# Performance work log

Hardware: AMD Instinct MI355X
Metric: run time of the kernel (lower is better)

Reference implementation:

```python
import jax, jax.numpy as jnp
import numpy as np

N, E, D, H, G, C = 100000, 1200000, 64, 64, 128, 10


def setup_inputs() -> dict:
    key = jax.random.key(0)
    ks = jax.random.split(key, 20)
    def lin(k, fin, fout):
        kw, kb = jax.random.split(k)
        s = 1.0 / np.sqrt(fin)
        return (jax.random.uniform(kw, (fin, fout), jnp.float32, -s, s),
                jax.random.uniform(kb, (fout,), jnp.float32, -s, s))
    w1a, b1a = lin(ks[0], D, H)
    w1b, b1b = lin(ks[1], H, H)
    w2a, b2a = lin(ks[2], H, H)
    w2b, b2b = lin(ks[3], H, H)
    w3a, b3a = lin(ks[4], H, H)
    w3b, b3b = lin(ks[5], H, H)
    wc, bc = lin(ks[6], H, C)
    x = jax.random.normal(ks[7], (N, D), jnp.float32)
    edge_index = jax.random.randint(ks[8], (2, E), 0, N, dtype=jnp.int32)
    batch = jnp.sort(jax.random.randint(ks[9], (N,), 0, G, dtype=jnp.int32))
    return {"x": x, "w1a": w1a, "b1a": b1a, "w1b": w1b, "b1b": b1b,
            "w2a": w2a, "b2a": b2a, "w2b": w2b, "b2b": b2b,
            "w3a": w3a, "b3a": b3a, "w3b": w3b, "b3b": b3b,
            "wc": wc, "bc": bc, "edge_index": edge_index, "batch": batch}


def _gin_layer(x, src, dst, wa, ba, wb, bb):
    # GINConv (eps=0): mlp(x + sum_{j in N(i)} x_j), then outer ReLU from GIN.forward
    agg = jax.ops.segment_sum(x[src], dst, num_segments=N)  # [N, d]
    h = x + agg
    h = jax.nn.relu(h @ wa + ba) @ wb + bb
    return jax.nn.relu(h)


def reference(x, w1a, b1a, w1b, b1b, w2a, b2a, w2b, b2b,
              w3a, b3a, w3b, b3b, wc, bc, edge_index, batch):
    src, dst = edge_index[0], edge_index[1]
    x = _gin_layer(x, src, dst, w1a, b1a, w1b, b1b)
    x = _gin_layer(x, src, dst, w2a, b2a, w2b, b2b)
    x = _gin_layer(x, src, dst, w3a, b3a, w3b, b3b)
    # global mean pool over graphs
    sums = jax.ops.segment_sum(x, batch, num_segments=G)              # [G, H]
    cnts = jax.ops.segment_sum(jnp.ones((N,), x.dtype), batch, num_segments=G)
    pooled = sums / jnp.maximum(cnts, 1.0)[:, None]
    return pooled @ wc + bc  # [G, C]
```

## Files before the change

### kernel.cpp

```cpp
#include <hip/hip_runtime.h>
#include <hip/hip_bf16.h>


#define N_NODES 100000
#define N_EDGES 1200000
#define N_GRAPH 128
#define N_CLS   10
#define NBUCK   391
#define BCAP    4096
#define BSH     12
#define HALFN   50000

typedef __bf16 bf16_t;
typedef __bf16 bf16x8 __attribute__((ext_vector_type(8)));
typedef float  f32x4  __attribute__((ext_vector_type(4)));

__global__ void tobf_kernel(const float* __restrict__ x, bf16_t* __restrict__ xb) {
    const int i = (blockIdx.x * 256 + threadIdx.x) * 8;
    const f32x4 a = *(const f32x4*)(x + i);
    const f32x4 b = *(const f32x4*)(x + i + 4);
    bf16x8 o;
#pragma unroll
    for (int j = 0; j < 4; ++j) { o[j] = (bf16_t)a[j]; o[4 + j] = (bf16_t)b[j]; }
    *(bf16x8*)(xb + i) = o;
}

__global__ void binA_kernel(const int* __restrict__ ei,
                            int* __restrict__ bcnt,
                            int* __restrict__ bpair) {
    __shared__ int lcnt[NBUCK];
    __shared__ int lbase[NBUCK];
    const int t = threadIdx.x;
    for (int b = t; b < NBUCK; b += 256) lcnt[b] = 0;
    __syncthreads();
    const int e0 = (blockIdx.x * 256 + t) * 4;
    int4 s4, d4; int b[4], r[4];
    const bool valid = e0 < N_EDGES;
    if (valid) {
        s4 = *(const int4*)(ei + e0);
        d4 = *(const int4*)(ei + N_EDGES + e0);
        b[0] = d4.x >> 8; b[1] = d4.y >> 8; b[2] = d4.z >> 8; b[3] = d4.w >> 8;
        r[0] = atomicAdd(&lcnt[b[0]], 1);
        r[1] = atomicAdd(&lcnt[b[1]], 1);
        r[2] = atomicAdd(&lcnt[b[2]], 1);
        r[3] = atomicAdd(&lcnt[b[3]], 1);
    }
    __syncthreads();
    for (int bb = t; bb < NBUCK; bb += 256) {
        const int c = lcnt[bb];
        lbase[bb] = c ? atomicAdd(&bcnt[bb], c) : 0;
    }
    __syncthreads();
    if (valid) {
        const int ss[4] = {s4.x, s4.y, s4.z, s4.w};
        const int dd[4] = {d4.x, d4.y, d4.z, d4.w};
#pragma unroll
        for (int j = 0; j < 4; ++j) {
            const int slot = lbase[b[j]] + r[j];
            if (slot < BCAP)
                bpair[(b[j] << BSH) + slot] = (ss[j] << 8) | (dd[j] & 255);
        }
    }
}

__global__ void bscan_kernel(const int* __restrict__ bcnt, int* __restrict__ cbase,
                             int* __restrict__ offset) {
    __shared__ int l[512];
    const int t = threadIdx.x;
    const int v = (t < NBUCK) ? bcnt[t] : 0;
    l[t] = v;
    __syncthreads();
    for (int d = 1; d < 512; d <<= 1) {
        int u = l[t];
        if (t >= d) u += l[t - d];
        __syncthreads();
        l[t] = u;
        __syncthreads();
    }
    if (t < NBUCK) cbase[t] = l[t] - v;
    if (t == NBUCK - 1) offset[N_NODES] = l[t];
}

__global__ void sortfill_kernel(const int* __restrict__ bpair,
                                const int* __restrict__ bcnt,
                                const int* __restrict__ cbase,
                                int* __restrict__ offset, int* __restrict__ csr) {
    __shared__ int hist[256];
    __shared__ int l[256];
    __shared__ int cursor[256];
    const int b = blockIdx.x;
    const int t = threadIdx.x;
    const int base = b << BSH;
    int cnt = bcnt[b];
    cnt = cnt < BCAP ? cnt : BCAP;

    hist[t] = 0;
    __syncthreads();
    for (int i = t; i < cnt; i += 256)
        atomicAdd(&hist[bpair[base + i] & 255], 1);
    __syncthreads();

    const int v = hist[t];
    l[t] = v;
    __syncthreads();
    for (int d = 1; d < 256; d <<= 1) {
        int u = l[t];
        if (t >= d) u += l[t - d];
        __syncthreads();
        l[t] = u;
        __syncthreads();
    }
    const int gpos = cbase[b] + l[t] - v;
    const int node = (b << 8) + t;
    if (node < N_NODES) offset[node] = gpos;
    cursor[t] = gpos;
    __syncthreads();

    for (int i = t; i < cnt; i += 256) {
        const int p = bpair[base + i];
        const int pos = atomicAdd(&cursor[p & 255], 1);
        csr[pos] = p >> 8;
    }
}

#define GATHER8(S, ACC)                                                        \
    {                                                                          \
        const int t0 = __shfl(S, j + 0), t1 = __shfl(S, j + 1);                \
        const int t2 = __shfl(S, j + 2), t3 = __shfl(S, j + 3);                \
        const int t4 = __shfl(S, j + 4), t5 = __shfl(S, j + 5);                \
        const int t6 = __shfl(S, j + 6), t7 = __shfl(S, j + 7);                \
        const float u0 = (float)x[t0 * 64 + f], u1 = (float)x[t1 * 64 + f];    \
        const float u2 = (float)x[t2 * 64 + f], u3 = (float)x[t3 * 64 + f];    \
        const float u4 = (float)x[t4 * 64 + f], u5 = (float)x[t5 * 64 + f];    \
        const float u6 = (float)x[t6 * 64 + f], u7 = (float)x[t7 * 64 + f];    \
        ACC += ((u0 + u1) + (u2 + u3)) + ((u4 + u5) + (u6 + u7));              \
    }
#define GATHER4(S, J, ACC)                                                     \
    {                                                                          \
        const int t0 = __shfl(S, J + 0), t1 = __shfl(S, J + 1);                \
        const int t2 = __shfl(S, J + 2), t3 = __shfl(S, J + 3);                \
        const float u0 = (float)x[t0 * 64 + f], u1 = (float)x[t1 * 64 + f];    \
        const float u2 = (float)x[t2 * 64 + f], u3 = (float)x[t3 * 64 + f];    \
        ACC += (u0 + u1) + (u2 + u3);                                          \
    }

__global__ void agg2_kernel(const bf16_t* __restrict__ x,
                            const int* __restrict__ offset,
                            const int* __restrict__ csr,
                            bf16_t* __restrict__ hout) {
    const int w = (blockIdx.x * 256 + threadIdx.x) >> 6;
    const int f = threadIdx.x & 63;
    const int nA = w;
    const int nB = w + HALFN;

    const int oA = offset[nA], eA = offset[nA + 1];
    const int oB = offset[nB], eB = offset[nB + 1];
    const int dA = eA - oA, dB = eB - oB;

    float accA = (float)x[nA * 64 + f];
    float accB = (float)x[nB * 64 + f];

    for (int base = 0; base < dA || base < dB; base += 64) {
        const int ra = dA - base, rb2 = dB - base;
        const int cntA = ra <= 0 ? 0 : (ra < 64 ? ra : 64);
        const int cntB = rb2 <= 0 ? 0 : (rb2 < 64 ? rb2 : 64);
        int sA = 0, sB = 0;
        if (f < cntA) sA = csr[oA + base + f];
        if (f < cntB) sB = csr[oB + base + f];

        int j = 0;
        for (; j + 8 <= cntA && j + 8 <= cntB; j += 8) {
            GATHER8(sA, accA)
            GATHER8(sB, accB)
        }
        int jA = j, jB = j;
        for (; jA + 8 <= cntA; jA += 8) { const int j = jA; GATHER8(sA, accA) }
        for (; jB + 8 <= cntB; jB += 8) { const int j = jB; GATHER8(sB, accB) }
        if (jA + 4 <= cntA && jB + 4 <= cntB) {
            GATHER4(sA, jA, accA)
            GATHER4(sB, jB, accB)
            jA += 4; jB += 4;
        }
        if (jA + 4 <= cntA) { GATHER4(sA, jA, accA) jA += 4; }
        if (jB + 4 <= cntB) { GATHER4(sB, jB, accB) jB += 4; }
        for (; jA < cntA; ++jA) { const int t = __shfl(sA, jA); accA += (float)x[t * 64 + f]; }
        for (; jB < cntB; ++jB) { const int t = __shfl(sB, jB); accB += (float)x[t * 64 + f]; }
    }
    hout[nA * 64 + f] = (bf16_t)accA;
    hout[nB * 64 + f] = (bf16_t)accB;
}

template <int POOL>
__global__ void mlp_kernel(const bf16_t* __restrict__ hin,
                           const float* __restrict__ wa, const float* __restrict__ ba,
                           const float* __restrict__ wb, const float* __restrict__ bb,
                           bf16_t* __restrict__ xout,
                           const int* __restrict__ batch,
                           float* __restrict__ gsum) {
    __shared__ __align__(16) bf16_t wfrag[2][8][64][8];
    __shared__ __align__(16) bf16_t hs[4][16][72];
    __shared__ float biasA[64], biasB[64];

    const int tid  = threadIdx.x;
    const int wv   = tid >> 6;
    const int lane = tid & 63;
    const int l15  = lane & 15;
    const int quad = lane >> 4;

    {
        const int k  = tid >> 2;
        const int n0 = (tid & 3) << 4;
        const int ks = k >> 5, qd = (k >> 3) & 3, jj = k & 7;
        const int fi = ((n0 >> 4) << 1) + ks;
#pragma unroll
        for (int m = 0; m < 2; ++m) {
            const float* w = m ? wb : wa;
            const f32x4 v0 = *(const f32x4*)(w + k * 64 + n0);
            const f32x4 v1 = *(const f32x4*)(w + k * 64 + n0 + 4);
            const f32x4 v2 = *(const f32x4*)(w + k * 64 + n0 + 8);
            const f32x4 v3 = *(const f32x4*)(w + k * 64 + n0 + 12);
#pragma unroll
            for (int l = 0; l < 4; ++l) {
                wfrag[m][fi][qd * 16 + l][jj]      = (bf16_t)v0[l];
                wfrag[m][fi][qd * 16 + 4 + l][jj]  = (bf16_t)v1[l];
                wfrag[m][fi][qd * 16 + 8 + l][jj]  = (bf16_t)v2[l];
                wfrag[m][fi][qd * 16 + 12 + l][jj] = (bf16_t)v3[l];
            }
        }
        if (tid < 64) biasA[tid] = ba[tid];
        else if (tid < 128) biasB[tid - 64] = bb[tid - 64];
    }
    __syncthreads();

    const int ntiles = (N_NODES + 63) / 64;
    for (int tile = blockIdx.x; tile < ntiles; tile += gridDim.x) {
        const int rb = tile * 64 + wv * 16;
        const int rowa = rb + l15;
        const int rowc = rowa < N_NODES ? rowa : N_NODES - 1;

        bf16x8 af[2];
#pragma unroll
        for (int ks = 0; ks < 2; ++ks)
            af[ks] = *(const bf16x8*)(hin + rowc * 64 + ks * 32 + quad * 8);

#pragma unroll
        for (int ct = 0; ct < 4; ++ct) {
            const bf16x8 b0 = *(const bf16x8*)&wfrag[0][ct * 2 + 0][lane][0];
            const bf16x8 b1 = *(const bf16x8*)&wfrag[0][ct * 2 + 1][lane][0];
            f32x4 acc = {0.f, 0.f, 0.f, 0.f};
            acc = __builtin_amdgcn_mfma_f32_16x16x32_bf16(af[0], b0, acc, 0, 0, 0);
            acc = __builtin_amdgcn_mfma_f32_16x16x32_bf16(af[1], b1, acc, 0, 0, 0);
            const float bv = biasA[ct * 16 + l15];
#pragma unroll
            for (int r = 0; r < 4; ++r) {
                float h = acc[r] + bv;
                h = h > 0.f ? h : 0.f;
                hs[wv][quad * 4 + r][ct * 16 + l15] = (bf16_t)h;
            }
        }

        bf16x8 a2[2];
#pragma unroll
        for (int ks = 0; ks < 2; ++ks)
            a2[ks] = *(const bf16x8*)(&hs[wv][l15][ks * 32 + quad * 8]);

#pragma unroll
        for (int ct = 0; ct < 4; ++ct) {
            const bf16x8 b0 = *(const bf16x8*)&wfrag[1][ct * 2 + 0][lane][0];
            const bf16x8 b1 = *(const bf16x8*)&wfrag[1][ct * 2 + 1][lane][0];
            f32x4 acc = {0.f, 0.f, 0.f, 0.f};
            acc = __builtin_amdgcn_mfma_f32_16x16x32_bf16(a2[0], b0, acc, 0, 0, 0);
            acc = __builtin_amdgcn_mfma_f32_16x16x32_bf16(a2[1], b1, acc, 0, 0, 0);
            const float bv = biasB[ct * 16 + l15];
#pragma unroll
            for (int r = 0; r < 4; ++r) {
                float h = acc[r] + bv;
                h = h > 0.f ? h : 0.f;
                hs[wv][quad * 4 + r][ct * 16 + l15] = (bf16_t)h;
            }
        }

        if (POOL) {
            int cur = -1;
            float acc = 0.f;
            for (int r = 0; r < 16; ++r) {
                const int row = rb + r;
                if (row >= N_NODES) break;
                const int g = batch[row];
                const float v = (float)hs[wv][r][lane];
                if (g != cur) {
                    if (cur >= 0) unsafeAtomicAdd(gsum + cur * 64 + lane, acc);
                    acc = 0.f;
                    cur = g;
                }
                acc += v;
            }
            if (cur >= 0) unsafeAtomicAdd(gsum + cur * 64 + lane, acc);
        } else {
            const int colg = (lane & 7) * 8;
#pragma unroll
            for (int sx = 0; sx < 2; ++sx) {
                const int r16 = (lane >> 3) + 8 * sx;
                const int grow = rb + r16;
                const bf16x8 v = *(const bf16x8*)&hs[wv][r16][colg];
                if (grow < N_NODES)
                    *(bf16x8*)(xout + grow * 64 + colg) = v;
            }
        }
    }
}

__global__ void cls_kernel(const float* __restrict__ gsum,
                           const int* __restrict__ batch,
                           const float* __restrict__ wc, const float* __restrict__ bc,
                           float* __restrict__ out) {
    const int g = blockIdx.x;
    const int c = threadIdx.x;
    if (c >= N_CLS) return;
    int lo = 0, hi = N_NODES;
    while (lo < hi) { const int m = (lo + hi) >> 1; if (batch[m] < g) lo = m + 1; else hi = m; }
    const int lb = lo;
    lo = 0; hi = N_NODES;
    while (lo < hi) { const int m = (lo + hi) >> 1; if (batch[m] <= g) lo = m + 1; else hi = m; }
    const int cnt = lo - lb;
    const float inv = 1.f / (float)(cnt > 1 ? cnt : 1);
    float acc = bc[c];
    for (int k = 0; k < 64; ++k)
        acc += gsum[g * 64 + k] * inv * wc[k * N_CLS + c];
    out[g * N_CLS + c] = acc;
}

extern "C" void kernel_launch(void* const* d_in, const int* in_sizes, int n_in,
                              void* d_out, int out_size, void* d_ws, size_t ws_size,
                              hipStream_t stream) {
    const float* x   = (const float*)d_in[0];
    const float* w1a = (const float*)d_in[1];
    const float* b1a = (const float*)d_in[2];
    const float* w1b = (const float*)d_in[3];
    const float* b1b = (const float*)d_in[4];
    const float* w2a = (const float*)d_in[5];
    const float* b2a = (const float*)d_in[6];
    const float* w2b = (const float*)d_in[7];
    const float* b2b = (const float*)d_in[8];
    const float* w3a = (const float*)d_in[9];
    const float* b3a = (const float*)d_in[10];
    const float* w3b = (const float*)d_in[11];
    const float* b3b = (const float*)d_in[12];
    const float* wc  = (const float*)d_in[13];
    const float* bc  = (const float*)d_in[14];
    const int*   ei    = (const int*)d_in[15];
    const int*   batch = (const int*)d_in[16];
    float* out = (float*)d_out;

    char*   ws     = (char*)d_ws;
    int*    bcnt   = (int*)ws;
    int*    cbase  = (int*)(ws + 1568);
    int*    offset = (int*)(ws + 3136);
    int*    csr    = (int*)(ws + 403152);
    int*    bpair  = (int*)(ws + 5203152);
    bf16_t* xbf    = (bf16_t*)(ws + 11609296);
    bf16_t* h      = (bf16_t*)(ws + 24409296);
    bf16_t* xA     = (bf16_t*)(ws + 37209296);
    float*  gsum   = (float*)(ws + 50009296);

    const int e4grid  = (N_EDGES / 4 + 255) / 256;
    const int a2grid  = HALFN / 4;
    const int mlpgrid = 782;

    tobf_kernel<<<(N_NODES * 64) / (256 * 8), 256, 0, stream>>>(x, xbf);

    hipMemsetAsync(bcnt, 0, 1568, stream);
    hipMemsetAsync(gsum, 0, 32768, stream);
    binA_kernel<<<e4grid, 256, 0, stream>>>(ei, bcnt, bpair);
    bscan_kernel<<<1, 512, 0, stream>>>(bcnt, cbase, offset);
    sortfill_kernel<<<NBUCK, 256, 0, stream>>>(bpair, bcnt, cbase, offset, csr);

    agg2_kernel<<<a2grid, 256, 0, stream>>>(xbf, offset, csr, h);
    mlp_kernel<0><<<mlpgrid, 256, 0, stream>>>(h, w1a, b1a, w1b, b1b, xA, nullptr, nullptr);
    agg2_kernel<<<a2grid, 256, 0, stream>>>(xA, offset, csr, h);
    mlp_kernel<0><<<mlpgrid, 256, 0, stream>>>(h, w2a, b2a, w2b, b2b, xA, nullptr, nullptr);
    agg2_kernel<<<a2grid, 256, 0, stream>>>(xA, offset, csr, h);
    mlp_kernel<1><<<mlpgrid, 256, 0, stream>>>(h, w3a, b3a, w3b, b3b, nullptr, batch, gsum);

    cls_kernel<<<N_GRAPH, 64, 0, stream>>>(gsum, batch, wc, bc, out);
}
```

Measured before the change: 329.8 us.

## Fuse memsets and bucket scan into neighboring kernels, prefetch MLP tiles

Zeroing of bucket counts and graph sums moves into the bf16 conversion kernel, replacing two memset calls. The single-block bucket scan kernel is removed; each sortfill block instead reduces the counts of the preceding buckets itself. The MLP kernel loads the next tile's input rows before computing the current tile. The aim is fewer launches and less serialization, at the cost of redundant prefix reductions per block and extra registers.

```diff
diff --git a/kernel.cpp b/kernel.cpp
--- a/kernel.cpp
+++ b/kernel.cpp
@@ -15,7 +15,15 @@
 typedef __bf16 bf16x8 __attribute__((ext_vector_type(8)));
 typedef float  f32x4  __attribute__((ext_vector_type(4)));
 
-__global__ void tobf_kernel(const float* __restrict__ x, bf16_t* __restrict__ xb) {
+__global__ void tobf_kernel(const float* __restrict__ x, bf16_t* __restrict__ xb,
+                            int* __restrict__ bcnt, float* __restrict__ gsum) {
+    if (blockIdx.x == 0) {
+        for (int i = threadIdx.x; i < NBUCK; i += 256) bcnt[i] = 0;
+    } else if (blockIdx.x == 1) {
+        f32x4* g4 = (f32x4*)gsum;
+        for (int i = threadIdx.x; i < N_GRAPH * 16; i += 256)
+            g4[i] = (f32x4){0.f, 0.f, 0.f, 0.f};
+    }
     const int i = (blockIdx.x * 256 + threadIdx.x) * 8;
     const f32x4 a = *(const f32x4*)(x + i);
     const f32x4 b = *(const f32x4*)(x + i + 4);
@@ -63,36 +71,33 @@
     }
 }
 
-__global__ void bscan_kernel(const int* __restrict__ bcnt, int* __restrict__ cbase,
-                             int* __restrict__ offset) {
-    __shared__ int l[512];
-    const int t = threadIdx.x;
-    const int v = (t < NBUCK) ? bcnt[t] : 0;
-    l[t] = v;
-    __syncthreads();
-    for (int d = 1; d < 512; d <<= 1) {
-        int u = l[t];
-        if (t >= d) u += l[t - d];
-        __syncthreads();
-        l[t] = u;
-        __syncthreads();
-    }
-    if (t < NBUCK) cbase[t] = l[t] - v;
-    if (t == NBUCK - 1) offset[N_NODES] = l[t];
-}
-
 __global__ void sortfill_kernel(const int* __restrict__ bpair,
                                 const int* __restrict__ bcnt,
-                                const int* __restrict__ cbase,
                                 int* __restrict__ offset, int* __restrict__ csr) {
+    __shared__ int red[256];
     __shared__ int hist[256];
     __shared__ int l[256];
     __shared__ int cursor[256];
     const int b = blockIdx.x;
     const int t = threadIdx.x;
     const int base = b << BSH;
+
+    int part = 0;
+    for (int i = t; i < b; i += 256) {
+        int c = bcnt[i];
+        part += (c < BCAP ? c : BCAP);
+    }
+    red[t] = part;
+    __syncthreads();
+    for (int d = 128; d > 0; d >>= 1) {
+        if (t < d) red[t] += red[t + d];
+        __syncthreads();
+    }
+    const int cbase = red[0];
     int cnt = bcnt[b];
     cnt = cnt < BCAP ? cnt : BCAP;
+    if (b == NBUCK - 1 && t == 0) offset[N_NODES] = cbase + cnt;
+    __syncthreads();
 
     hist[t] = 0;
     __syncthreads();
@@ -110,7 +115,7 @@
         l[t] = u;
         __syncthreads();
     }
-    const int gpos = cbase[b] + l[t] - v;
+    const int gpos = cbase + l[t] - v;
     const int node = (b << 8) + t;
     if (node < N_NODES) offset[node] = gpos;
     cursor[t] = gpos;
@@ -233,15 +238,31 @@
     __syncthreads();
 
     const int ntiles = (N_NODES + 63) / 64;
-    for (int tile = blockIdx.x; tile < ntiles; tile += gridDim.x) {
-        const int rb = tile * 64 + wv * 16;
-        const int rowa = rb + l15;
+    int tile = blockIdx.x;
+
+    bf16x8 af[2];
+    {
+        const int rowa = tile * 64 + wv * 16 + l15;
         const int rowc = rowa < N_NODES ? rowa : N_NODES - 1;
-
-        bf16x8 af[2];
 #pragma unroll
         for (int ks = 0; ks < 2; ++ks)
             af[ks] = *(const bf16x8*)(hin + rowc * 64 + ks * 32 + quad * 8);
+    }
+
+    for (;;) {
+        const int next = tile + gridDim.x;
+        const bool has_next = next < ntiles;
+
+        bf16x8 afn[2];
+        if (has_next) {
+            const int rowa = next * 64 + wv * 16 + l15;
+            const int rowc = rowa < N_NODES ? rowa : N_NODES - 1;
+#pragma unroll
+            for (int ks = 0; ks < 2; ++ks)
+                afn[ks] = *(const bf16x8*)(hin + rowc * 64 + ks * 32 + quad * 8);
+        }
+
+        const int rb = tile * 64 + wv * 16;
 
 #pragma unroll
         for (int ct = 0; ct < 4; ++ct) {
@@ -307,6 +328,11 @@
                     *(bf16x8*)(xout + grow * 64 + colg) = v;
             }
         }
+
+        if (!has_next) break;
+        af[0] = afn[0];
+        af[1] = afn[1];
+        tile = next;
     }
 }
 
@@ -354,7 +380,6 @@
 
     char*   ws     = (char*)d_ws;
     int*    bcnt   = (int*)ws;
-    int*    cbase  = (int*)(ws + 1568);
     int*    offset = (int*)(ws + 3136);
     int*    csr    = (int*)(ws + 403152);
     int*    bpair  = (int*)(ws + 5203152);
@@ -367,13 +392,10 @@
     const int a2grid  = HALFN / 4;
     const int mlpgrid = 782;
 
-    tobf_kernel<<<(N_NODES * 64) / (256 * 8), 256, 0, stream>>>(x, xbf);
-
-    hipMemsetAsync(bcnt, 0, 1568, stream);
-    hipMemsetAsync(gsum, 0, 32768, stream);
+    tobf_kernel<<<(N_NODES * 64) / (256 * 8), 256, 0, stream>>>(x, xbf, bcnt, gsum);
+
     binA_kernel<<<e4grid, 256, 0, stream>>>(ei, bcnt, bpair);
-    bscan_kernel<<<1, 512, 0, stream>>>(bcnt, cbase, offset);
-    sortfill_kernel<<<NBUCK, 256, 0, stream>>>(bpair, bcnt, cbase, offset, csr);
+    sortfill_kernel<<<NBUCK, 256, 0, stream>>>(bpair, bcnt, offset, csr);
 
     agg2_kernel<<<a2grid, 256, 0, stream>>>(xbf, offset, csr, h);
     mlp_kernel<0><<<mlpgrid, 256, 0, stream>>>(h, w1a, b1a, w1b, b1b, xA, nullptr, nullptr);
```

Measured after the change: 323.2 us. 1.02x faster.
